# Performance work log

Hardware: AMD Instinct MI355X
Metric: run time of the kernel (lower is better)

Reference implementation:

```python
import jax, jax.numpy as jnp
import numpy as np

D_MODEL = 768
HIDDEN = 2048  # round(768*8/3)=2048, already a multiple of 64
N_EXPERTS = 8
ALPHA = 0.05  # load_balance_alpha


def setup_inputs() -> dict:
    key = jax.random.key(0)
    k0, k1, k2, k3, k4 = jax.random.split(key, 5)
    x = jax.random.normal(k0, (2, 2048, D_MODEL), dtype=jnp.float32)
    wg_w = jax.random.normal(k1, (N_EXPERTS, D_MODEL), dtype=jnp.float32) * 0.02
    wg_b = jnp.zeros((N_EXPERTS,), dtype=jnp.float32)
    Wu = jax.random.normal(k2, (N_EXPERTS, D_MODEL, HIDDEN), dtype=jnp.float32) * 0.02
    Wv = jax.random.normal(k3, (N_EXPERTS, D_MODEL, HIDDEN), dtype=jnp.float32) * 0.02
    Wd = jax.random.normal(k4, (N_EXPERTS, HIDDEN, D_MODEL), dtype=jnp.float32) * 0.02
    return {"x": x, "wg_w": wg_w, "wg_b": wg_b, "Wu": Wu, "Wv": Wv, "Wd": Wd}


def reference(x, wg_w, wg_b, Wu, Wv, Wd):
    b, t, d = x.shape
    xf = x.reshape(b * t, d)  # [N, d]

    # ---- Top1Router (eval mode: temp=1, no noise, z_loss_coef=0) ----
    logits = xf @ wg_w.T + wg_b            # [N, E]
    probs = jax.nn.softmax(logits, axis=-1)
    top1_idx = jnp.argmax(logits, axis=-1)  # [N]
    top1_p = jnp.take_along_axis(probs, top1_idx[:, None], axis=1)[:, 0]  # [N]

    # aux loss: me and ce computed under no_grad in the torch source -> stop_gradient
    one_hot = jax.nn.one_hot(top1_idx, N_EXPERTS, dtype=probs.dtype)
    me = jax.lax.stop_gradient(one_hot.mean(axis=0))   # [E]
    ce = jax.lax.stop_gradient(probs.mean(axis=0))     # [E]
    aux = ALPHA * N_EXPERTS * jnp.sum(me * ce)

    # ---- Dropless dispatch: per-expert masked SwiGLU, combined with top1 gate ----
    gate = top1_p[:, None]  # [N, 1]
    y = jnp.zeros_like(xf)
    for e in range(N_EXPERTS):
        mask = (top1_idx == e)[:, None]            # [N, 1]
        xe = jnp.where(mask, xf, 0.0)              # zero-out non-routed tokens (no biases -> exact)
        u = xe @ Wu[e]                              # [N, H]
        v = xe @ Wv[e]                              # [N, H]
        ye = (jax.nn.silu(u) * v) @ Wd[e]           # [N, d]
        y = y + jnp.where(mask, ye * gate, 0.0)
    return y.reshape(b, t, d), aux
```

## Files before the change

### kernel.cpp

```cpp
#include <hip/hip_runtime.h>
#include <cstdint>
#include <cstddef>

#define TOK 4096
#define DM 768
#define HID 2048
#define NE 8

typedef __attribute__((ext_vector_type(8))) short bf16x8;
typedef __attribute__((ext_vector_type(4))) float f32x4;

__device__ __forceinline__ unsigned short f2bf(float f) {
  unsigned int u = __float_as_uint(f);
  u += 0x7FFF + ((u >> 16) & 1);
  return (unsigned short)(u >> 16);
}

__global__ __launch_bounds__(256)
void k_gate(const float* __restrict__ x, const float* __restrict__ wgw,
            const float* __restrict__ wgb,
            int* __restrict__ eidx, float* __restrict__ gatep,
            int* __restrict__ pos, int* __restrict__ counts,
            float* __restrict__ ce_partial)
{
  __shared__ float ce_loc[4][NE];
  const int lane = threadIdx.x & 63;
  const int w = threadIdx.x >> 6;
  const int t = blockIdx.x * 4 + w;

  float acc[NE];
#pragma unroll
  for (int e = 0; e < NE; ++e) acc[e] = 0.f;
  const float* xr = x + (size_t)t * DM;
#pragma unroll
  for (int j = 0; j < DM / 64; ++j) {
    float xv = xr[j * 64 + lane];
#pragma unroll
    for (int e = 0; e < NE; ++e) acc[e] += xv * wgw[e * DM + j * 64 + lane];
  }
#pragma unroll
  for (int e = 0; e < NE; ++e) {
    float v = acc[e];
#pragma unroll
    for (int off = 32; off >= 1; off >>= 1) v += __shfl_xor(v, off);
    acc[e] = v + wgb[e];
  }
  float mx = acc[0]; int ai = 0;
#pragma unroll
  for (int e = 1; e < NE; ++e) if (acc[e] > mx) { mx = acc[e]; ai = e; }
  float p[NE]; float se = 0.f;
#pragma unroll
  for (int e = 0; e < NE; ++e) { p[e] = expf(acc[e] - mx); se += p[e]; }
  float inv = 1.f / se;

  if (lane == 0) {
#pragma unroll
    for (int e = 0; e < NE; ++e) ce_loc[w][e] = p[e] * inv;
    eidx[t] = ai;
    gatep[t] = p[ai] * inv;
    pos[t] = atomicAdd(&counts[ai], 1);
  }
  __syncthreads();
  if (threadIdx.x < NE) {
    float s = ce_loc[0][threadIdx.x] + ce_loc[1][threadIdx.x]
            + ce_loc[2][threadIdx.x] + ce_loc[3][threadIdx.x];
    ce_partial[blockIdx.x * NE + threadIdx.x] = s;
  }
}

__global__ __launch_bounds__(256)
void k_reduce(const int* __restrict__ counts, const float* __restrict__ cepart,
              int* __restrict__ offs, float* __restrict__ aux_out)
{
  __shared__ float sl[256][NE];
  const int tid = threadIdx.x;
  float s[NE];
#pragma unroll
  for (int e = 0; e < NE; ++e) s[e] = 0.f;
  for (int b = tid; b < TOK / 4; b += 256)
#pragma unroll
    for (int e = 0; e < NE; ++e) s[e] += cepart[b * NE + e];
#pragma unroll
  for (int e = 0; e < NE; ++e) sl[tid][e] = s[e];
  __syncthreads();
  for (int st = 128; st > 0; st >>= 1) {
    if (tid < st)
#pragma unroll
      for (int e = 0; e < NE; ++e) sl[tid][e] += sl[tid + st][e];
    __syncthreads();
  }
  if (tid == 0) {
    int o = 0;
    for (int e = 0; e < NE; ++e) { offs[e] = o; o += counts[e]; }
    offs[NE] = o;
    float aux = 0.f;
    for (int e = 0; e < NE; ++e)
      aux += ((float)counts[e] / 4096.f) * (sl[0][e] / 4096.f);
    aux_out[0] = 0.05f * 8.f * aux;
  }
}

__global__ __launch_bounds__(256)
void k_scatter(const float* __restrict__ x, const int* __restrict__ eidx,
               const float* __restrict__ gatep, const int* __restrict__ pos,
               const int* __restrict__ offs, int* __restrict__ tlist,
               float* __restrict__ gate_b, unsigned short* __restrict__ xb)
{
  const int lane = threadIdx.x & 63;
  const int w = threadIdx.x >> 6;
  const int t = blockIdx.x * 4 + w;
  const int e = eidx[t];
  const int row = offs[e] + pos[t];
  if (lane == 0) { tlist[row] = t; gate_b[row] = gatep[t]; }
  const float4* src = (const float4*)(x + (size_t)t * DM);
  uint2* dst = (uint2*)(xb + (size_t)row * DM);
#pragma unroll
  for (int c = 0; c < 3; ++c) {
    float4 v = src[lane + c * 64];
    uint2 d;
    d.x = (unsigned)f2bf(v.x) | ((unsigned)f2bf(v.y) << 16);
    d.y = (unsigned)f2bf(v.z) | ((unsigned)f2bf(v.w) << 16);
    dst[lane + c * 64] = d;
  }
}

__global__ __launch_bounds__(256, 2)
void k_ffn1(const float* __restrict__ Wu, const float* __restrict__ Wv,
            const unsigned short* __restrict__ xb, const float* __restrict__ gate_b,
            const int* __restrict__ offs, unsigned short* __restrict__ h)
{
  const int e = blockIdx.z;
  const int m0 = offs[e];
  const int Me = offs[e + 1] - m0;
  const int tm = blockIdx.y;
  if (tm * 128 >= Me) return;
  const int tn = blockIdx.x;

  __shared__ __align__(16) unsigned short As[4096];
  __shared__ __align__(16) unsigned short Bus[4096];
  __shared__ __align__(16) unsigned short Bvs[4096];

  const int tid = threadIdx.x;
  const int lane = tid & 63;
  const int wm = (tid >> 6) >> 1;
  const int wn = (tid >> 6) & 1;

  f32x4 accU[4][4], accV[4][4];
#pragma unroll
  for (int i = 0; i < 4; ++i)
#pragma unroll
    for (int j = 0; j < 4; ++j)
#pragma unroll
      for (int k = 0; k < 4; ++k) { accU[i][j][k] = 0.f; accV[i][j][k] = 0.f; }

  const unsigned short* xrow0 = xb + (size_t)(m0 + tm * 128) * DM;
  const float* wu0 = Wu + (size_t)e * DM * HID + tn * 128;
  const float* wv0 = Wv + (size_t)e * DM * HID + tn * 128;

  const int am0 = tid >> 2, ako = tid & 3;
  const int bn = tid & 127, bko0 = tid >> 7;

  for (int kt = 0; kt < DM / 32; ++kt) {
#pragma unroll
    for (int s = 0; s < 2; ++s) {
      int m = am0 + s * 64;
      uint4 av = *(const uint4*)(xrow0 + (size_t)m * DM + kt * 32 + ako * 8);
      *(uint4*)&As[(m >> 4) * 512 + ((m & 15) + ako * 16) * 8] = av;
    }
#pragma unroll
    for (int s = 0; s < 2; ++s) {
      int ko = bko0 + s * 2;
      int krow = kt * 32 + ko * 8;
      const float* pu = wu0 + (size_t)krow * HID + bn;
      const float* pv = wv0 + (size_t)krow * HID + bn;
      unsigned int du[4], dv[4];
#pragma unroll
      for (int jj = 0; jj < 4; ++jj) {
        du[jj] = (unsigned)f2bf(pu[(size_t)(2 * jj) * HID]) |
                 ((unsigned)f2bf(pu[(size_t)(2 * jj + 1) * HID]) << 16);
        dv[jj] = (unsigned)f2bf(pv[(size_t)(2 * jj) * HID]) |
                 ((unsigned)f2bf(pv[(size_t)(2 * jj + 1) * HID]) << 16);
      }
      int base = (bn >> 4) * 512 + ((bn & 15) + ko * 16) * 8;
      uint4 uu; uu.x = du[0]; uu.y = du[1]; uu.z = du[2]; uu.w = du[3];
      uint4 vv; vv.x = dv[0]; vv.y = dv[1]; vv.z = dv[2]; vv.w = dv[3];
      *(uint4*)&Bus[base] = uu;
      *(uint4*)&Bvs[base] = vv;
    }
    __syncthreads();
    bf16x8 a[4], bu[4], bv[4];
#pragma unroll
    for (int i = 0; i < 4; ++i) a[i] = *(const bf16x8*)&As[(wm * 4 + i) * 512 + lane * 8];
#pragma unroll
    for (int j = 0; j < 4; ++j) {
      bu[j] = *(const bf16x8*)&Bus[(wn * 4 + j) * 512 + lane * 8];
      bv[j] = *(const bf16x8*)&Bvs[(wn * 4 + j) * 512 + lane * 8];
    }
#pragma unroll
    for (int i = 0; i < 4; ++i)
#pragma unroll
      for (int j = 0; j < 4; ++j) {
        accU[i][j] = __builtin_amdgcn_mfma_f32_16x16x32_bf16(a[i], bu[j], accU[i][j], 0, 0, 0);
        accV[i][j] = __builtin_amdgcn_mfma_f32_16x16x32_bf16(a[i], bv[j], accV[i][j], 0, 0, 0);
      }
    __syncthreads();
  }
  const int colbase = tn * 128 + wn * 64;
  const int rlane = (lane >> 4) * 4;
  const int clane = lane & 15;
#pragma unroll
  for (int i = 0; i < 4; ++i) {
#pragma unroll
    for (int r = 0; r < 4; ++r) {
      int rowIn = wm * 64 + i * 16 + rlane + r;
      if (tm * 128 + rowIn < Me) {
        int grow = m0 + tm * 128 + rowIn;
        float g = gate_b[grow];
        unsigned short* hp = h + (size_t)grow * HID + colbase + clane;
#pragma unroll
        for (int j = 0; j < 4; ++j) {
          float u_ = accU[i][j][r];
          float v_ = accV[i][j][r];
          float sv = u_ / (1.f + expf(-u_));
          hp[j * 16] = f2bf(sv * v_ * g);
        }
      }
    }
  }
}

__global__ __launch_bounds__(256, 2)
void k_ffn2(const float* __restrict__ Wd, const unsigned short* __restrict__ h,
            const int* __restrict__ offs, const int* __restrict__ tlist,
            float* __restrict__ y)
{
  const int tn = blockIdx.x;
  if (tn >= 6) return;
  const int e = blockIdx.z;
  const int m0 = offs[e];
  const int Me = offs[e + 1] - m0;
  const int tm = blockIdx.y;
  if (tm * 64 >= Me) return;

  __shared__ __align__(16) unsigned short As[2048];
  __shared__ __align__(16) unsigned short Bs[4096];

  const int tid = threadIdx.x;
  const int lane = tid & 63;
  const int wm = (tid >> 6) >> 1;
  const int wn = (tid >> 6) & 1;

  f32x4 acc[2][4];
#pragma unroll
  for (int i = 0; i < 2; ++i)
#pragma unroll
    for (int j = 0; j < 4; ++j)
#pragma unroll
      for (int k = 0; k < 4; ++k) acc[i][j][k] = 0.f;

  const unsigned short* hrow0 = h + (size_t)(m0 + tm * 64) * HID;
  const float* wd0 = Wd + (size_t)e * HID * DM + tn * 128;

  const int am = tid >> 2, ako = tid & 3;
  const int bn = tid & 127, bko0 = tid >> 7;

  for (int kt = 0; kt < HID / 32; ++kt) {
    uint4 av = *(const uint4*)(hrow0 + (size_t)am * HID + kt * 32 + ako * 8);
    *(uint4*)&As[(am >> 4) * 512 + ((am & 15) + ako * 16) * 8] = av;
#pragma unroll
    for (int s = 0; s < 2; ++s) {
      int ko = bko0 + s * 2;
      int krow = kt * 32 + ko * 8;
      const float* pb = wd0 + (size_t)krow * DM + bn;
      unsigned int d[4];
#pragma unroll
      for (int jj = 0; jj < 4; ++jj)
        d[jj] = (unsigned)f2bf(pb[(size_t)(2 * jj) * DM]) |
                ((unsigned)f2bf(pb[(size_t)(2 * jj + 1) * DM]) << 16);
      uint4 bb; bb.x = d[0]; bb.y = d[1]; bb.z = d[2]; bb.w = d[3];
      *(uint4*)&Bs[(bn >> 4) * 512 + ((bn & 15) + ko * 16) * 8] = bb;
    }
    __syncthreads();
    bf16x8 a[2], b[4];
#pragma unroll
    for (int i = 0; i < 2; ++i) a[i] = *(const bf16x8*)&As[(wm * 2 + i) * 512 + lane * 8];
#pragma unroll
    for (int j = 0; j < 4; ++j) b[j] = *(const bf16x8*)&Bs[(wn * 4 + j) * 512 + lane * 8];
#pragma unroll
    for (int i = 0; i < 2; ++i)
#pragma unroll
      for (int j = 0; j < 4; ++j)
        acc[i][j] = __builtin_amdgcn_mfma_f32_16x16x32_bf16(a[i], b[j], acc[i][j], 0, 0, 0);
    __syncthreads();
  }
  const int colbase = tn * 128 + wn * 64;
  const int rlane = (lane >> 4) * 4;
  const int clane = lane & 15;
#pragma unroll
  for (int i = 0; i < 2; ++i) {
#pragma unroll
    for (int r = 0; r < 4; ++r) {
      int rowIn = wm * 32 + i * 16 + rlane + r;
      if (tm * 64 + rowIn < Me) {
        int tok = tlist[m0 + tm * 64 + rowIn];
        float* yp = y + (size_t)tok * DM + colbase + clane;
#pragma unroll
        for (int j = 0; j < 4; ++j) yp[j * 16] = acc[i][j][r];
      }
    }
  }
}

extern "C" void kernel_launch(void* const* d_in, const int* in_sizes, int n_in,
                              void* d_out, int out_size, void* d_ws, size_t ws_size,
                              hipStream_t stream)
{
  const float* x   = (const float*)d_in[0];
  const float* wgw = (const float*)d_in[1];
  const float* wgb = (const float*)d_in[2];
  const float* Wu  = (const float*)d_in[3];
  const float* Wv  = (const float*)d_in[4];
  const float* Wd  = (const float*)d_in[5];
  float* out = (float*)d_out;

  char* ws = (char*)d_ws;
  int*   eidx   = (int*)(ws + 0);
  float* gatep  = (float*)(ws + 16384);
  int*   pos    = (int*)(ws + 32768);
  int*   counts = (int*)(ws + 49152);
  int*   offs   = (int*)(ws + 49216);
  float* cepart = (float*)(ws + 49664);
  int*   tlist  = (int*)(ws + 82432);
  float* gate_b = (float*)(ws + 98816);
  unsigned short* xb = (unsigned short*)(ws + 115712);
  unsigned short* h  = (unsigned short*)(ws + 6603776);

  hipMemsetAsync(counts, 0, 64, stream);
  k_gate<<<TOK / 4, 256, 0, stream>>>(x, wgw, wgb, eidx, gatep, pos, counts, cepart);
  k_reduce<<<1, 256, 0, stream>>>(counts, cepart, offs, out + (size_t)TOK * DM);
  k_scatter<<<TOK / 4, 256, 0, stream>>>(x, eidx, gatep, pos, offs, tlist, gate_b, xb);
  k_ffn1<<<dim3(16, 32, 8), 256, 0, stream>>>(Wu, Wv, xb, gate_b, offs, h);
  k_ffn2<<<dim3(8, 64, 8), 256, 0, stream>>>(Wd, h, offs, tlist, out);
}
```

Before: 415.7 us.

## Pre-convert weights to swizzled bf16 tiles, use async LDS loads, split-K ffn2

Weight conversion from fp32 to a pre-tiled, XOR-swizzled bf16 layout now happens once per call inside the gating kernel, so the GEMM kernels no longer do strided fp32 loads and conversion in their inner loops. Tokens are scattered into expert regions padded to 128 rows and laid out as tiles. The FFN kernels stage tiles with global_load_lds async copies. ffn2 switches to 128-row tiles with a 4-way split-K and atomic accumulation into a zeroed output. Kernels are merged from five to four launches, at the cost of extra workspace, a full pass over all weights each call, and atomic-add traffic with nondeterministic summation order.

```diff
diff --git a/kernel.cpp b/kernel.cpp
--- a/kernel.cpp
+++ b/kernel.cpp
@@ -10,140 +10,201 @@
 typedef __attribute__((ext_vector_type(8))) short bf16x8;
 typedef __attribute__((ext_vector_type(4))) float f32x4;
 
+#define ASYNC16(GP, LP) \
+  __builtin_amdgcn_global_load_lds((__attribute__((address_space(1))) void*)(GP), \
+                                   (__attribute__((address_space(3))) void*)(LP), 16, 0, 0)
+
 __device__ __forceinline__ unsigned short f2bf(float f) {
   unsigned int u = __float_as_uint(f);
   u += 0x7FFF + ((u >> 16) & 1);
   return (unsigned short)(u >> 16);
 }
+__device__ __forceinline__ unsigned int pack2(float a, float b) {
+  return (unsigned)f2bf(a) | ((unsigned)f2bf(b) << 16);
+}
+__device__ __forceinline__ int padded_off(const int* counts, int e) {
+  int o = 0;
+  for (int i = 0; i < e; ++i) o += (counts[i] + 127) & ~127;
+  return o;
+}
+
 
 __global__ __launch_bounds__(256)
-void k_gate(const float* __restrict__ x, const float* __restrict__ wgw,
-            const float* __restrict__ wgb,
-            int* __restrict__ eidx, float* __restrict__ gatep,
-            int* __restrict__ pos, int* __restrict__ counts,
-            float* __restrict__ ce_partial)
+void k1_gate_convert(const float* __restrict__ x, const float* __restrict__ wgw,
+                     const float* __restrict__ wgb,
+                     const float* __restrict__ Wu, const float* __restrict__ Wv,
+                     const float* __restrict__ Wd,
+                     int* __restrict__ eidx, float* __restrict__ gatep,
+                     int* __restrict__ pos, int* __restrict__ counts,
+                     float* __restrict__ cepart,
+                     unsigned short* __restrict__ wub, unsigned short* __restrict__ wvb,
+                     unsigned short* __restrict__ wdb)
 {
   __shared__ float ce_loc[4][NE];
-  const int lane = threadIdx.x & 63;
-  const int w = threadIdx.x >> 6;
-  const int t = blockIdx.x * 4 + w;
-
-  float acc[NE];
-#pragma unroll
-  for (int e = 0; e < NE; ++e) acc[e] = 0.f;
-  const float* xr = x + (size_t)t * DM;
-#pragma unroll
-  for (int j = 0; j < DM / 64; ++j) {
-    float xv = xr[j * 64 + lane];
-#pragma unroll
-    for (int e = 0; e < NE; ++e) acc[e] += xv * wgw[e * DM + j * 64 + lane];
-  }
-#pragma unroll
-  for (int e = 0; e < NE; ++e) {
-    float v = acc[e];
-#pragma unroll
-    for (int off = 32; off >= 1; off >>= 1) v += __shfl_xor(v, off);
-    acc[e] = v + wgb[e];
-  }
-  float mx = acc[0]; int ai = 0;
-#pragma unroll
-  for (int e = 1; e < NE; ++e) if (acc[e] > mx) { mx = acc[e]; ai = e; }
-  float p[NE]; float se = 0.f;
-#pragma unroll
-  for (int e = 0; e < NE; ++e) { p[e] = expf(acc[e] - mx); se += p[e]; }
-  float inv = 1.f / se;
-
-  if (lane == 0) {
-#pragma unroll
-    for (int e = 0; e < NE; ++e) ce_loc[w][e] = p[e] * inv;
-    eidx[t] = ai;
-    gatep[t] = p[ai] * inv;
-    pos[t] = atomicAdd(&counts[ai], 1);
-  }
-  __syncthreads();
-  if (threadIdx.x < NE) {
-    float s = ce_loc[0][threadIdx.x] + ce_loc[1][threadIdx.x]
-            + ce_loc[2][threadIdx.x] + ce_loc[3][threadIdx.x];
-    ce_partial[blockIdx.x * NE + threadIdx.x] = s;
+  const int b = blockIdx.x;
+  if (b < 1024) {
+    const int lane = threadIdx.x & 63;
+    const int w = threadIdx.x >> 6;
+    const int t = b * 4 + w;
+    float acc[NE];
+#pragma unroll
+    for (int e = 0; e < NE; ++e) acc[e] = 0.f;
+    const float* xr = x + (size_t)t * DM;
+#pragma unroll
+    for (int j = 0; j < DM / 64; ++j) {
+      float xv = xr[j * 64 + lane];
+#pragma unroll
+      for (int e = 0; e < NE; ++e) acc[e] += xv * wgw[e * DM + j * 64 + lane];
+    }
+#pragma unroll
+    for (int e = 0; e < NE; ++e) {
+      float v = acc[e];
+#pragma unroll
+      for (int off = 32; off >= 1; off >>= 1) v += __shfl_xor(v, off);
+      acc[e] = v + wgb[e];
+    }
+    float mx = acc[0]; int ai = 0;
+#pragma unroll
+    for (int e = 1; e < NE; ++e) if (acc[e] > mx) { mx = acc[e]; ai = e; }
+    float p[NE]; float se = 0.f;
+#pragma unroll
+    for (int e = 0; e < NE; ++e) { p[e] = expf(acc[e] - mx); se += p[e]; }
+    float inv = 1.f / se;
+    if (lane == 0) {
+#pragma unroll
+      for (int e = 0; e < NE; ++e) ce_loc[w][e] = p[e] * inv;
+      eidx[t] = ai;
+      gatep[t] = p[ai] * inv;
+      pos[t] = atomicAdd(&counts[ai], 1);
+    }
+    __syncthreads();
+    if (threadIdx.x < NE) {
+      float s = ce_loc[0][threadIdx.x] + ce_loc[1][threadIdx.x]
+              + ce_loc[2][threadIdx.x] + ce_loc[3][threadIdx.x];
+      cepart[b * NE + threadIdx.x] = s;
+    }
+    return;
+  }
+  const int cb = b - 1024;
+  const int seg = cb / 3072;
+  const int r = cb % 3072;
+  const int e = r / 384;
+  const int rem = r % 384;
+  const float* W;
+  unsigned short* blob;
+  int N, nt, kt;
+  if (seg < 2) {
+    N = HID; nt = rem / 24; kt = rem % 24;
+    W = (seg == 0) ? Wu : Wv;
+    blob = ((seg == 0) ? wub : wvb) + (size_t)((e * 16 + nt) * 24 + kt) * 4096;
+    W += (size_t)e * DM * HID;
+  } else {
+    N = DM; nt = rem / 64; kt = rem % 64;
+    W = Wd + (size_t)e * HID * DM;
+    blob = wdb + (size_t)((e * 6 + nt) * 64 + kt) * 4096;
+  }
+  const int t = threadIdx.x;
+#pragma unroll
+  for (int c = 0; c < 2; ++c) {
+    const int unit = c * 256 + t;
+    const int nl = unit >> 2, s = unit & 3, ko = s ^ (nl & 3);
+    const float* src = W + (size_t)(kt * 32 + ko * 8) * N + nt * 128 + nl;
+    uint4 u;
+    u.x = pack2(src[0], src[(size_t)N]);
+    u.y = pack2(src[(size_t)2 * N], src[(size_t)3 * N]);
+    u.z = pack2(src[(size_t)4 * N], src[(size_t)5 * N]);
+    u.w = pack2(src[(size_t)6 * N], src[(size_t)7 * N]);
+    *(uint4*)(blob + (size_t)unit * 8) = u;
   }
 }
 
 __global__ __launch_bounds__(256)
-void k_reduce(const int* __restrict__ counts, const float* __restrict__ cepart,
-              int* __restrict__ offs, float* __restrict__ aux_out)
+void k2_scatter_zero_aux(const float* __restrict__ x, const int* __restrict__ eidx,
+                         const float* __restrict__ gatep, const int* __restrict__ pos,
+                         const int* __restrict__ counts, const float* __restrict__ cepart,
+                         int* __restrict__ tlist, float* __restrict__ gate_b,
+                         unsigned short* __restrict__ xb,
+                         float* __restrict__ y, float* __restrict__ aux_out)
 {
   __shared__ float sl[256][NE];
-  const int tid = threadIdx.x;
-  float s[NE];
-#pragma unroll
-  for (int e = 0; e < NE; ++e) s[e] = 0.f;
-  for (int b = tid; b < TOK / 4; b += 256)
-#pragma unroll
-    for (int e = 0; e < NE; ++e) s[e] += cepart[b * NE + e];
-#pragma unroll
-  for (int e = 0; e < NE; ++e) sl[tid][e] = s[e];
-  __syncthreads();
-  for (int st = 128; st > 0; st >>= 1) {
-    if (tid < st)
-#pragma unroll
-      for (int e = 0; e < NE; ++e) sl[tid][e] += sl[tid + st][e];
-    __syncthreads();
-  }
-  if (tid == 0) {
-    int o = 0;
-    for (int e = 0; e < NE; ++e) { offs[e] = o; o += counts[e]; }
-    offs[NE] = o;
-    float aux = 0.f;
-    for (int e = 0; e < NE; ++e)
-      aux += ((float)counts[e] / 4096.f) * (sl[0][e] / 4096.f);
-    aux_out[0] = 0.05f * 8.f * aux;
-  }
-}
-
-__global__ __launch_bounds__(256)
-void k_scatter(const float* __restrict__ x, const int* __restrict__ eidx,
-               const float* __restrict__ gatep, const int* __restrict__ pos,
-               const int* __restrict__ offs, int* __restrict__ tlist,
-               float* __restrict__ gate_b, unsigned short* __restrict__ xb)
-{
-  const int lane = threadIdx.x & 63;
-  const int w = threadIdx.x >> 6;
-  const int t = blockIdx.x * 4 + w;
-  const int e = eidx[t];
-  const int row = offs[e] + pos[t];
-  if (lane == 0) { tlist[row] = t; gate_b[row] = gatep[t]; }
-  const float4* src = (const float4*)(x + (size_t)t * DM);
-  uint2* dst = (uint2*)(xb + (size_t)row * DM);
-#pragma unroll
-  for (int c = 0; c < 3; ++c) {
-    float4 v = src[lane + c * 64];
-    uint2 d;
-    d.x = (unsigned)f2bf(v.x) | ((unsigned)f2bf(v.y) << 16);
-    d.y = (unsigned)f2bf(v.z) | ((unsigned)f2bf(v.w) << 16);
-    dst[lane + c * 64] = d;
+  const int b = blockIdx.x;
+  if (b < 1024) {
+    const int lane = threadIdx.x & 63;
+    const int w = threadIdx.x >> 6;
+    const int t = b * 4 + w;
+    const int e = eidx[t];
+    const int prow = padded_off(counts, e) + pos[t];
+    if (lane == 0) { tlist[prow] = t; gate_b[prow] = gatep[t]; }
+    const int tile = prow >> 7, m = prow & 127;
+    const float* xr = x + (size_t)t * DM;
+#pragma unroll
+    for (int c = 0; c < 2; ++c) {
+      int u = c * 64 + lane;
+      if (u < 96) {
+        int kt = u >> 2, ko = u & 3;
+        const float4* s4 = (const float4*)(xr + kt * 32 + ko * 8);
+        float4 v0 = s4[0], v1 = s4[1];
+        uint4 d;
+        d.x = pack2(v0.x, v0.y); d.y = pack2(v0.z, v0.w);
+        d.z = pack2(v1.x, v1.y); d.w = pack2(v1.z, v1.w);
+        int slot = m * 4 + (ko ^ (m & 3));
+        *(uint4*)(xb + ((size_t)(tile * 24 + kt) * 512 + slot) * 8) = d;
+      }
+    }
+  } else if (b < 1536) {
+    float4* y4 = (float4*)y;
+    const int base = (b - 1024) * 1536 + threadIdx.x;
+#pragma unroll
+    for (int c = 0; c < 6; ++c) {
+      float4 z; z.x = 0.f; z.y = 0.f; z.z = 0.f; z.w = 0.f;
+      y4[base + c * 256] = z;
+    }
+  } else {
+    const int tid = threadIdx.x;
+    float s[NE];
+#pragma unroll
+    for (int e = 0; e < NE; ++e) s[e] = 0.f;
+    for (int bb = tid; bb < 1024; bb += 256)
+#pragma unroll
+      for (int e = 0; e < NE; ++e) s[e] += cepart[bb * NE + e];
+#pragma unroll
+    for (int e = 0; e < NE; ++e) sl[tid][e] = s[e];
+    __syncthreads();
+    for (int st = 128; st > 0; st >>= 1) {
+      if (tid < st)
+#pragma unroll
+        for (int e = 0; e < NE; ++e) sl[tid][e] += sl[tid + st][e];
+      __syncthreads();
+    }
+    if (tid == 0) {
+      float aux = 0.f;
+      for (int e = 0; e < NE; ++e)
+        aux += ((float)counts[e] / 4096.f) * (sl[0][e] / 4096.f);
+      aux_out[0] = 0.05f * 8.f * aux;
+    }
   }
 }
 
 __global__ __launch_bounds__(256, 2)
-void k_ffn1(const float* __restrict__ Wu, const float* __restrict__ Wv,
+void k_ffn1(const unsigned short* __restrict__ wub, const unsigned short* __restrict__ wvb,
             const unsigned short* __restrict__ xb, const float* __restrict__ gate_b,
-            const int* __restrict__ offs, unsigned short* __restrict__ h)
+            const int* __restrict__ counts, unsigned short* __restrict__ h)
 {
   const int e = blockIdx.z;
-  const int m0 = offs[e];
-  const int Me = offs[e + 1] - m0;
+  const int Me = counts[e];
   const int tm = blockIdx.y;
   if (tm * 128 >= Me) return;
   const int tn = blockIdx.x;
-
-  __shared__ __align__(16) unsigned short As[4096];
-  __shared__ __align__(16) unsigned short Bus[4096];
-  __shared__ __align__(16) unsigned short Bvs[4096];
+  const int prowbase = padded_off(counts, e) + tm * 128;
+  const int atile = prowbase >> 7;
+
+  __shared__ __align__(16) unsigned short Sh[12288];
 
   const int tid = threadIdx.x;
   const int lane = tid & 63;
-  const int wm = (tid >> 6) >> 1;
-  const int wn = (tid >> 6) & 1;
+  const int wv_ = tid >> 6;
+  const int wm = wv_ >> 1, wn = wv_ & 1;
+  const int wu_id = __builtin_amdgcn_readfirstlane(wv_);
 
   f32x4 accU[4][4], accV[4][4];
 #pragma unroll
@@ -153,48 +214,37 @@
 #pragma unroll
       for (int k = 0; k < 4; ++k) { accU[i][j][k] = 0.f; accV[i][j][k] = 0.f; }
 
-  const unsigned short* xrow0 = xb + (size_t)(m0 + tm * 128) * DM;
-  const float* wu0 = Wu + (size_t)e * DM * HID + tn * 128;
-  const float* wv0 = Wv + (size_t)e * DM * HID + tn * 128;
-
-  const int am0 = tid >> 2, ako = tid & 3;
-  const int bn = tid & 127, bko0 = tid >> 7;
-
-  for (int kt = 0; kt < DM / 32; ++kt) {
-#pragma unroll
-    for (int s = 0; s < 2; ++s) {
-      int m = am0 + s * 64;
-      uint4 av = *(const uint4*)(xrow0 + (size_t)m * DM + kt * 32 + ako * 8);
-      *(uint4*)&As[(m >> 4) * 512 + ((m & 15) + ako * 16) * 8] = av;
-    }
-#pragma unroll
-    for (int s = 0; s < 2; ++s) {
-      int ko = bko0 + s * 2;
-      int krow = kt * 32 + ko * 8;
-      const float* pu = wu0 + (size_t)krow * HID + bn;
-      const float* pv = wv0 + (size_t)krow * HID + bn;
-      unsigned int du[4], dv[4];
-#pragma unroll
-      for (int jj = 0; jj < 4; ++jj) {
-        du[jj] = (unsigned)f2bf(pu[(size_t)(2 * jj) * HID]) |
-                 ((unsigned)f2bf(pu[(size_t)(2 * jj + 1) * HID]) << 16);
-        dv[jj] = (unsigned)f2bf(pv[(size_t)(2 * jj) * HID]) |
-                 ((unsigned)f2bf(pv[(size_t)(2 * jj + 1) * HID]) << 16);
-      }
-      int base = (bn >> 4) * 512 + ((bn & 15) + ko * 16) * 8;
-      uint4 uu; uu.x = du[0]; uu.y = du[1]; uu.z = du[2]; uu.w = du[3];
-      uint4 vv; vv.x = dv[0]; vv.y = dv[1]; vv.z = dv[2]; vv.w = dv[3];
-      *(uint4*)&Bus[base] = uu;
-      *(uint4*)&Bvs[base] = vv;
+  const char* AbBase = (const char*)xb + ((size_t)(atile * 24) << 13);
+  const char* BuBase = (const char*)wub + ((size_t)((e * 16 + tn) * 24) << 13);
+  const char* BvBase = (const char*)wvb + ((size_t)((e * 16 + tn) * 24) << 13);
+  const int lc = lane & 15, q = lane >> 4;
+
+  for (int kt = 0; kt < 24; ++kt) {
+    const char* Ab = AbBase + ((size_t)kt << 13);
+    const char* Bub = BuBase + ((size_t)kt << 13);
+    const char* Bvb = BvBase + ((size_t)kt << 13);
+#pragma unroll
+    for (int c2 = 0; c2 < 6; ++c2) {
+      const int c = wu_id * 6 + c2;
+      const char* g;
+      if (c < 8)       g = Ab + c * 1024 + lane * 16;
+      else if (c < 16) g = Bub + (c - 8) * 1024 + lane * 16;
+      else             g = Bvb + (c - 16) * 1024 + lane * 16;
+      ASYNC16(g, (char*)Sh + (unsigned)(c * 1024));
     }
     __syncthreads();
     bf16x8 a[4], bu[4], bv[4];
 #pragma unroll
-    for (int i = 0; i < 4; ++i) a[i] = *(const bf16x8*)&As[(wm * 4 + i) * 512 + lane * 8];
+    for (int i = 0; i < 4; ++i) {
+      int m = wm * 64 + i * 16 + lc;
+      a[i] = *(const bf16x8*)&Sh[(m * 4 + (q ^ (m & 3))) * 8];
+    }
 #pragma unroll
     for (int j = 0; j < 4; ++j) {
-      bu[j] = *(const bf16x8*)&Bus[(wn * 4 + j) * 512 + lane * 8];
-      bv[j] = *(const bf16x8*)&Bvs[(wn * 4 + j) * 512 + lane * 8];
+      int n = wn * 64 + j * 16 + lc;
+      int slb = (n * 4 + (q ^ (n & 3))) * 8;
+      bu[j] = *(const bf16x8*)&Sh[4096 + slb];
+      bv[j] = *(const bf16x8*)&Sh[8192 + slb];
     }
 #pragma unroll
     for (int i = 0; i < 4; ++i)
@@ -214,9 +264,9 @@
     for (int r = 0; r < 4; ++r) {
       int rowIn = wm * 64 + i * 16 + rlane + r;
       if (tm * 128 + rowIn < Me) {
-        int grow = m0 + tm * 128 + rowIn;
-        float g = gate_b[grow];
-        unsigned short* hp = h + (size_t)grow * HID + colbase + clane;
+        int prow = prowbase + rowIn;
+        float g = gate_b[prow];
+        unsigned short* hp = h + (size_t)prow * HID + colbase + clane;
 #pragma unroll
         for (int j = 0; j < 4; ++j) {
           float u_ = accU[i][j][r];
@@ -230,82 +280,86 @@
 }
 
 __global__ __launch_bounds__(256, 2)
-void k_ffn2(const float* __restrict__ Wd, const unsigned short* __restrict__ h,
-            const int* __restrict__ offs, const int* __restrict__ tlist,
+void k_ffn2(const unsigned short* __restrict__ wdb, const unsigned short* __restrict__ h,
+            const int* __restrict__ counts, const int* __restrict__ tlist,
             float* __restrict__ y)
 {
+  const int z = blockIdx.z;
+  const int e = z >> 2, split = z & 3;
+  const int Me = counts[e];
+  const int tm = blockIdx.y;
+  if (tm * 128 >= Me) return;
   const int tn = blockIdx.x;
-  if (tn >= 6) return;
-  const int e = blockIdx.z;
-  const int m0 = offs[e];
-  const int Me = offs[e + 1] - m0;
-  const int tm = blockIdx.y;
-  if (tm * 64 >= Me) return;
-
-  __shared__ __align__(16) unsigned short As[2048];
-  __shared__ __align__(16) unsigned short Bs[4096];
+  const int prowbase = padded_off(counts, e) + tm * 128;
+
+  __shared__ __align__(16) unsigned short Sh[8192];
 
   const int tid = threadIdx.x;
   const int lane = tid & 63;
-  const int wm = (tid >> 6) >> 1;
-  const int wn = (tid >> 6) & 1;
-
-  f32x4 acc[2][4];
-#pragma unroll
-  for (int i = 0; i < 2; ++i)
+  const int wv_ = tid >> 6;
+  const int wm = wv_ >> 1, wn = wv_ & 1;
+  const int wu_id = __builtin_amdgcn_readfirstlane(wv_);
+
+  f32x4 acc[4][4];
+#pragma unroll
+  for (int i = 0; i < 4; ++i)
 #pragma unroll
     for (int j = 0; j < 4; ++j)
 #pragma unroll
       for (int k = 0; k < 4; ++k) acc[i][j][k] = 0.f;
 
-  const unsigned short* hrow0 = h + (size_t)(m0 + tm * 64) * HID;
-  const float* wd0 = Wd + (size_t)e * HID * DM + tn * 128;
-
-  const int am = tid >> 2, ako = tid & 3;
-  const int bn = tid & 127, bko0 = tid >> 7;
-
-  for (int kt = 0; kt < HID / 32; ++kt) {
-    uint4 av = *(const uint4*)(hrow0 + (size_t)am * HID + kt * 32 + ako * 8);
-    *(uint4*)&As[(am >> 4) * 512 + ((am & 15) + ako * 16) * 8] = av;
-#pragma unroll
-    for (int s = 0; s < 2; ++s) {
-      int ko = bko0 + s * 2;
-      int krow = kt * 32 + ko * 8;
-      const float* pb = wd0 + (size_t)krow * DM + bn;
-      unsigned int d[4];
-#pragma unroll
-      for (int jj = 0; jj < 4; ++jj)
-        d[jj] = (unsigned)f2bf(pb[(size_t)(2 * jj) * DM]) |
-                ((unsigned)f2bf(pb[(size_t)(2 * jj + 1) * DM]) << 16);
-      uint4 bb; bb.x = d[0]; bb.y = d[1]; bb.z = d[2]; bb.w = d[3];
-      *(uint4*)&Bs[(bn >> 4) * 512 + ((bn & 15) + ko * 16) * 8] = bb;
-    }
-    __syncthreads();
-    bf16x8 a[2], b[4];
-#pragma unroll
-    for (int i = 0; i < 2; ++i) a[i] = *(const bf16x8*)&As[(wm * 2 + i) * 512 + lane * 8];
-#pragma unroll
-    for (int j = 0; j < 4; ++j) b[j] = *(const bf16x8*)&Bs[(wn * 4 + j) * 512 + lane * 8];
-#pragma unroll
-    for (int i = 0; i < 2; ++i)
+  const char* hB = (const char*)h + (size_t)prowbase * (HID * 2);
+  const char* BdBase = (const char*)wdb + ((size_t)((e * 6 + tn) * 64) << 13);
+  const int lc = lane & 15, q = lane >> 4;
+
+  for (int kti = 0; kti < 16; ++kti) {
+    const int ktg = split * 16 + kti;
+    const char* Bb = BdBase + ((size_t)ktg << 13);
+#pragma unroll
+    for (int c2 = 0; c2 < 4; ++c2) {
+      const int c = wu_id * 4 + c2;
+      const char* g;
+      if (c < 8) {
+        int mrow = c * 16 + (lane >> 2);
+        int ko = (lane & 3) ^ (mrow & 3);
+        g = hB + (size_t)mrow * (HID * 2) + ktg * 64 + ko * 16;
+      } else {
+        g = Bb + (c - 8) * 1024 + lane * 16;
+      }
+      ASYNC16(g, (char*)Sh + (unsigned)(c * 1024));
+    }
+    __syncthreads();
+    bf16x8 a[4], bfr[4];
+#pragma unroll
+    for (int i = 0; i < 4; ++i) {
+      int m = wm * 64 + i * 16 + lc;
+      a[i] = *(const bf16x8*)&Sh[(m * 4 + (q ^ (m & 3))) * 8];
+    }
+#pragma unroll
+    for (int j = 0; j < 4; ++j) {
+      int n = wn * 64 + j * 16 + lc;
+      bfr[j] = *(const bf16x8*)&Sh[4096 + (n * 4 + (q ^ (n & 3))) * 8];
+    }
+#pragma unroll
+    for (int i = 0; i < 4; ++i)
 #pragma unroll
       for (int j = 0; j < 4; ++j)
-        acc[i][j] = __builtin_amdgcn_mfma_f32_16x16x32_bf16(a[i], b[j], acc[i][j], 0, 0, 0);
+        acc[i][j] = __builtin_amdgcn_mfma_f32_16x16x32_bf16(a[i], bfr[j], acc[i][j], 0, 0, 0);
     __syncthreads();
   }
   const int colbase = tn * 128 + wn * 64;
   const int rlane = (lane >> 4) * 4;
   const int clane = lane & 15;
 #pragma unroll
-  for (int i = 0; i < 2; ++i) {
+  for (int i = 0; i < 4; ++i) {
 #pragma unroll
     for (int r = 0; r < 4; ++r) {
-      int rowIn = wm * 32 + i * 16 + rlane + r;
-      if (tm * 64 + rowIn < Me) {
-        int tok = tlist[m0 + tm * 64 + rowIn];
+      int rowIn = wm * 64 + i * 16 + rlane + r;
+      if (tm * 128 + rowIn < Me) {
+        int tok = tlist[prowbase + rowIn];
         float* yp = y + (size_t)tok * DM + colbase + clane;
 #pragma unroll
-        for (int j = 0; j < 4; ++j) yp[j * 16] = acc[i][j][r];
+        for (int j = 0; j < 4; ++j) atomicAdd(&yp[j * 16], acc[i][j][r]);
       }
     }
   }
@@ -324,21 +378,26 @@
   float* out = (float*)d_out;
 
   char* ws = (char*)d_ws;
-  int*   eidx   = (int*)(ws + 0);
-  float* gatep  = (float*)(ws + 16384);
-  int*   pos    = (int*)(ws + 32768);
-  int*   counts = (int*)(ws + 49152);
-  int*   offs   = (int*)(ws + 49216);
-  float* cepart = (float*)(ws + 49664);
-  int*   tlist  = (int*)(ws + 82432);
-  float* gate_b = (float*)(ws + 98816);
-  unsigned short* xb = (unsigned short*)(ws + 115712);
-  unsigned short* h  = (unsigned short*)(ws + 6603776);
-
-  hipMemsetAsync(counts, 0, 64, stream);
-  k_gate<<<TOK / 4, 256, 0, stream>>>(x, wgw, wgb, eidx, gatep, pos, counts, cepart);
-  k_reduce<<<1, 256, 0, stream>>>(counts, cepart, offs, out + (size_t)TOK * DM);
-  k_scatter<<<TOK / 4, 256, 0, stream>>>(x, eidx, gatep, pos, offs, tlist, gate_b, xb);
-  k_ffn1<<<dim3(16, 32, 8), 256, 0, stream>>>(Wu, Wv, xb, gate_b, offs, h);
-  k_ffn2<<<dim3(8, 64, 8), 256, 0, stream>>>(Wd, h, offs, tlist, out);
-}
+  int*   counts = (int*)(ws + 0);
+  int*   eidx   = (int*)(ws + 256);
+  float* gatep  = (float*)(ws + 16640);
+  int*   pos    = (int*)(ws + 33024);
+  float* cepart = (float*)(ws + 49408);
+  int*   tlist  = (int*)(ws + 82176);
+  float* gate_b = (float*)(ws + 102656);
+  unsigned short* xb  = (unsigned short*)(ws + 123136);
+  unsigned short* h   = (unsigned short*)(ws + 7987456);
+  unsigned short* wub = (unsigned short*)(ws + 28958976);
+  unsigned short* wvb = (unsigned short*)(ws + 54124800);
+  unsigned short* wdb = (unsigned short*)(ws + 79290624);
+
+  hipMemsetAsync(counts, 0, 32, stream);
+  k1_gate_convert<<<10240, 256, 0, stream>>>(x, wgw, wgb, Wu, Wv, Wd,
+                                             eidx, gatep, pos, counts, cepart,
+                                             wub, wvb, wdb);
+  k2_scatter_zero_aux<<<1537, 256, 0, stream>>>(x, eidx, gatep, pos, counts, cepart,
+                                                tlist, gate_b, xb,
+                                                out, out + (size_t)TOK * DM);
+  k_ffn1<<<dim3(16, 32, 8), 256, 0, stream>>>(wub, wvb, xb, gate_b, counts, h);
+  k_ffn2<<<dim3(6, 32, 32), 256, 0, stream>>>(wdb, h, counts, tlist, out);
+}
```

Measured after the change: 378.9 us. 1.1x faster.
